# Kernel optimization log

Hardware: AMD Instinct MI355X
Metric: run time of the kernel (lower is better)

## Reference

```python
import jax, jax.numpy as jnp
import numpy as np

MAX_STEP = 20

def setup_inputs() -> dict:
    key = jax.random.key(0)
    k1, k2 = jax.random.split(key)
    B, L, E, H = 32, 2048, 256, 256
    word_rep = jax.random.normal(k1, (B, L, E), dtype=jnp.float32)
    # nn.Parameter(torch.randn(...).uniform_(-0.1, 0.1)) -> uniform in [-0.1, 0.1]
    cnn = jax.random.uniform(k2, (MAX_STEP, E, H), dtype=jnp.float32, minval=-0.1, maxval=0.1)
    return {"word_rep": word_rep, "cnn": cnn}

def reference(word_rep, cnn):
    # word_rep: [B, L, E]; cnn: [MAX_STEP, E, H]
    L = word_rep.shape[1]
    # Gather the cyclically-indexed per-position weight: [L, E, H]
    W = cnn[jnp.arange(L) % MAX_STEP]
    # Fused batched matmul over all positions at once: [B, L, H]
    hidden_vecs = jnp.einsum('ble,leh->blh', word_rep, W)
    return (hidden_vecs, hidden_vecs[:, -1])
```

## Files before the change

### kernel.cpp

```cpp
#include <hip/hip_runtime.h>
#include <hip/hip_bf16.h>

#define B_ 32
#define L_ 2048
#define E_ 256
#define H_ 256
#define MAXSTEP 20
#define NL 4
#define NCH 26
#define NGRP (MAXSTEP * NCH)

typedef __attribute__((ext_vector_type(4))) float f32x4;
typedef __attribute__((ext_vector_type(8))) short bf16x8;
using bf16 = __hip_bfloat16;

__device__ inline short cvt1(float x) {
    bf16 b = __float2bfloat16(x);
    return *reinterpret_cast<short*>(&b);
}

__global__ void transpose_w_kernel(const float* __restrict__ cnn, short* __restrict__ wt) {
    __shared__ short tile[32][33];
    const int s  = blockIdx.z;
    const int e0 = blockIdx.y * 32;
    const int h0 = blockIdx.x * 32;
    const int tx = threadIdx.x;
    const int ty = threadIdx.y;
    const float* src = cnn + ((size_t)s * E_ + e0) * H_ + h0;
#pragma unroll
    for (int i = ty; i < 32; i += 8)
        tile[i][tx] = cvt1(src[(size_t)i * H_ + tx]);
    __syncthreads();
    short* dst = wt + ((size_t)s * H_ + h0) * E_ + e0;
#pragma unroll
    for (int i = ty; i < 32; i += 8)
        dst[(size_t)i * E_ + tx] = tile[tx][i];
}

__global__ __launch_bounds__(512, 4) void vaw_occ_kernel(
        const float* __restrict__ A, const short* __restrict__ Wt,
        float* __restrict__ out) {
    __shared__ __align__(16) float aLds[2][B_ * E_];

    const int g_    = blockIdx.x;
    const int s     = g_ / NCH;
    const int chunk = g_ % NCH;
    const int cnt   = (s < 8) ? 103 : 102;
    const int wv    = threadIdx.x >> 6;
    const int lane  = threadIdx.x & 63;
    const int r     = lane & 15;
    const int g     = lane >> 4;
    const int nbase = wv * 32;
    const int key   = r & 7;

    auto lof = [&](int il) {
        int idx = chunk * NL + il;
        if (idx > cnt - 1) idx = cnt - 1;
        return s + 20 * idx;
    };

    auto stage = [&](int it) {
        const int l = lof(it);
        float* dst = aLds[it & 1];
#pragma unroll
        for (int j = 0; j < 4; ++j) {
            const int row = wv + j * 8;
            const int cg  = lane ^ (row & 7);
            const float* gp = A + ((size_t)row * L_ + l) * E_ + cg * 4;
            __builtin_amdgcn_global_load_lds(
                (const __attribute__((address_space(1))) void*)gp,
                (__attribute__((address_space(3))) void*)&dst[row * 256],
                16, 0, 0);
        }
    };

    stage(0);
    stage(1);

    const short* wtb = Wt + ((size_t)s * H_ + nbase + r) * E_ + g * 8;
    bf16x8 breg[8][2];
#pragma unroll
    for (int kk = 0; kk < 8; ++kk)
#pragma unroll
        for (int nf = 0; nf < 2; ++nf)
            breg[kk][nf] = *(const bf16x8*)(wtb + (size_t)nf * 16 * E_ + kk * 32);

#pragma unroll 1
    for (int it = 0; it < NL; ++it) {
        const int l   = lof(it);
        const int cur = it & 1;

        if (it < NL - 1 && it >= 1) stage(it + 1);

        if (it < NL - 1) asm volatile("s_waitcnt vmcnt(20)" ::: "memory");
        else             asm volatile("s_waitcnt vmcnt(16)" ::: "memory");
        __builtin_amdgcn_s_barrier();
        __builtin_amdgcn_sched_barrier(0);

        f32x4 acc[2][2];
#pragma unroll
        for (int mf = 0; mf < 2; ++mf)
#pragma unroll
            for (int nf = 0; nf < 2; ++nf)
                acc[mf][nf] = f32x4{0.f, 0.f, 0.f, 0.f};

#pragma unroll
        for (int kk = 0; kk < 8; ++kk) {
            const int c0 = kk * 8 + g * 2;
            f32x4 a0lo = *(const f32x4*)&aLds[cur][r * 256 + ((c0 ^ key) << 2)];
            f32x4 a0hi = *(const f32x4*)&aLds[cur][r * 256 + (((c0 + 1) ^ key) << 2)];
            f32x4 a1lo = *(const f32x4*)&aLds[cur][(r + 16) * 256 + ((c0 ^ key) << 2)];
            f32x4 a1hi = *(const f32x4*)&aLds[cur][(r + 16) * 256 + (((c0 + 1) ^ key) << 2)];
            bf16x8 a0, a1;
#pragma unroll
            for (int j = 0; j < 4; ++j) {
                a0[j]     = cvt1(a0lo[j]);
                a0[j + 4] = cvt1(a0hi[j]);
                a1[j]     = cvt1(a1lo[j]);
                a1[j + 4] = cvt1(a1hi[j]);
            }
#pragma unroll
            for (int nf = 0; nf < 2; ++nf) {
                acc[0][nf] = __builtin_amdgcn_mfma_f32_16x16x32_bf16(a0, breg[kk][nf], acc[0][nf], 0, 0, 0);
                acc[1][nf] = __builtin_amdgcn_mfma_f32_16x16x32_bf16(a1, breg[kk][nf], acc[1][nf], 0, 0, 0);
            }
        }

        const int row0 = g * 4;
#pragma unroll
        for (int mf = 0; mf < 2; ++mf) {
#pragma unroll
            for (int nf = 0; nf < 2; ++nf) {
                const int h = nbase + nf * 16 + r;
#pragma unroll
                for (int i = 0; i < 4; ++i) {
                    const int bb = mf * 16 + row0 + i;
                    out[((size_t)bb * L_ + l) * H_ + h] = acc[mf][nf][i];
                }
            }
        }
        if (l == L_ - 1) {
            float* out2 = out + (size_t)B_ * L_ * H_;
#pragma unroll
            for (int mf = 0; mf < 2; ++mf)
#pragma unroll
                for (int nf = 0; nf < 2; ++nf) {
                    const int h = nbase + nf * 16 + r;
#pragma unroll
                    for (int i = 0; i < 4; ++i) {
                        const int bb = mf * 16 + row0 + i;
                        out2[(size_t)bb * H_ + h] = acc[mf][nf][i];
                    }
                }
        }

        __builtin_amdgcn_s_barrier();
    }
}

__global__ __launch_bounds__(256) void vaw_fallback_kernel(
        const float* __restrict__ A, const float* __restrict__ W, float* __restrict__ out) {
    __shared__ __align__(16) float aLds[2][B_ * E_];
    const int l0   = blockIdx.x * 4;
    const int wv   = threadIdx.x >> 6;
    const int lane = threadIdx.x & 63;
    const int r    = lane & 15;
    const int g    = lane >> 4;
    const int nbase = wv * 64;
    const int key   = r & 7;

    auto stage = [&](int it) {
        float* dst = aLds[it & 1];
        const int l = l0 + it;
#pragma unroll
        for (int t = 0; t < 8; ++t) {
            const int b  = t * 4 + wv;
            const int cgx = lane ^ (b & 7);
            const float* gp = A + ((size_t)b * L_ + l) * E_ + cgx * 4;
            __builtin_amdgcn_global_load_lds(
                (const __attribute__((address_space(1))) void*)gp,
                (__attribute__((address_space(3))) void*)&dst[b * 256],
                16, 0, 0);
        }
    };

    stage(0);
#pragma unroll 1
    for (int it = 0; it < 4; ++it) {
        const int l   = l0 + it;
        const int sidx = l % MAXSTEP;
        const int cur = it & 1;
        if (it < 3) {
            stage(it + 1);
            asm volatile("s_waitcnt vmcnt(8)" ::: "memory");
        } else {
            asm volatile("s_waitcnt vmcnt(0)" ::: "memory");
        }
        __builtin_amdgcn_s_barrier();
        __builtin_amdgcn_sched_barrier(0);

        f32x4 acc[2][4] = {};
        const float* Wf = W + (size_t)sidx * E_ * H_;
#pragma unroll 2
        for (int kk = 0; kk < 8; ++kk) {
            const int k0 = kk * 32;
            const int c0 = kk * 8 + g * 2;
            f32x4 a0lo = *(const f32x4*)&aLds[cur][r * 256 + ((c0 ^ key) << 2)];
            f32x4 a0hi = *(const f32x4*)&aLds[cur][r * 256 + (((c0 + 1) ^ key) << 2)];
            f32x4 a1lo = *(const f32x4*)&aLds[cur][(r + 16) * 256 + ((c0 ^ key) << 2)];
            f32x4 a1hi = *(const f32x4*)&aLds[cur][(r + 16) * 256 + (((c0 + 1) ^ key) << 2)];
            bf16x8 a0, a1;
#pragma unroll
            for (int j = 0; j < 4; ++j) {
                a0[j]     = cvt1(a0lo[j]);
                a0[j + 4] = cvt1(a0hi[j]);
                a1[j]     = cvt1(a1lo[j]);
                a1[j + 4] = cvt1(a1hi[j]);
            }
            bf16x8 b0, b1, b2, b3;
#pragma unroll
            for (int j = 0; j < 8; ++j) {
                const size_t krow = (size_t)(k0 + g * 8 + j) * H_;
                b0[j] = cvt1(Wf[krow + nbase +  0 + r]);
                b1[j] = cvt1(Wf[krow + nbase + 16 + r]);
                b2[j] = cvt1(Wf[krow + nbase + 32 + r]);
                b3[j] = cvt1(Wf[krow + nbase + 48 + r]);
            }
            acc[0][0] = __builtin_amdgcn_mfma_f32_16x16x32_bf16(a0, b0, acc[0][0], 0, 0, 0);
            acc[0][1] = __builtin_amdgcn_mfma_f32_16x16x32_bf16(a0, b1, acc[0][1], 0, 0, 0);
            acc[0][2] = __builtin_amdgcn_mfma_f32_16x16x32_bf16(a0, b2, acc[0][2], 0, 0, 0);
            acc[0][3] = __builtin_amdgcn_mfma_f32_16x16x32_bf16(a0, b3, acc[0][3], 0, 0, 0);
            acc[1][0] = __builtin_amdgcn_mfma_f32_16x16x32_bf16(a1, b0, acc[1][0], 0, 0, 0);
            acc[1][1] = __builtin_amdgcn_mfma_f32_16x16x32_bf16(a1, b1, acc[1][1], 0, 0, 0);
            acc[1][2] = __builtin_amdgcn_mfma_f32_16x16x32_bf16(a1, b2, acc[1][2], 0, 0, 0);
            acc[1][3] = __builtin_amdgcn_mfma_f32_16x16x32_bf16(a1, b3, acc[1][3], 0, 0, 0);
        }

        const int row0 = g * 4;
#pragma unroll
        for (int mf = 0; mf < 2; ++mf)
#pragma unroll
            for (int nf = 0; nf < 4; ++nf) {
                const int h = nbase + nf * 16 + r;
#pragma unroll
                for (int i = 0; i < 4; ++i) {
                    const int bb = mf * 16 + row0 + i;
                    out[((size_t)bb * L_ + l) * H_ + h] = acc[mf][nf][i];
                }
            }
        if (l == L_ - 1) {
            float* out2 = out + (size_t)B_ * L_ * H_;
#pragma unroll
            for (int mf = 0; mf < 2; ++mf)
#pragma unroll
                for (int nf = 0; nf < 4; ++nf) {
                    const int h = nbase + nf * 16 + r;
#pragma unroll
                    for (int i = 0; i < 4; ++i) {
                        const int bb = mf * 16 + row0 + i;
                        out2[(size_t)bb * H_ + h] = acc[mf][nf][i];
                    }
                }
        }
        __builtin_amdgcn_s_barrier();
    }
}

extern "C" void kernel_launch(void* const* d_in, const int* in_sizes, int n_in,
                              void* d_out, int out_size, void* d_ws, size_t ws_size,
                              hipStream_t stream) {
    const float* word_rep = (const float*)d_in[0];
    const float* cnn      = (const float*)d_in[1];
    float* out = (float*)d_out;

    const size_t wt_bytes = (size_t)MAXSTEP * E_ * H_ * sizeof(short);
    if (ws_size >= wt_bytes) {
        short* wt = (short*)d_ws;
        transpose_w_kernel<<<dim3(8, 8, 20), dim3(32, 8), 0, stream>>>(cnn, wt);
        vaw_occ_kernel<<<dim3(NGRP), dim3(512), 0, stream>>>(word_rep, wt, out);
    } else {
        vaw_fallback_kernel<<<dim3(L_ / 4), dim3(256), 0, stream>>>(word_rep, cnn, out);
    }
}
```

Baseline: 55.85 us.

## Swap MFMA operands for vectorized output stores and use 4-wave blocks

Passes the weight fragment as the first MFMA operand and the activation as the second, so each lane's accumulator holds four consecutive H values and results can be written as 16-byte vector stores instead of scalar strided stores. Blocks shrink from 8 waves to 4, and each wave now covers 64 output columns, which doubles the weight registers held per wave. Weight register loads move ahead of the activation staging, and only one stage is issued up front, with prefetch of the next stage inside the loop. The trade-off is higher register pressure and fewer waves per block, in exchange for coalesced output writes.

```diff
diff --git a/kernel.cpp b/kernel.cpp
--- a/kernel.cpp
+++ b/kernel.cpp
@@ -37,7 +37,7 @@
         dst[(size_t)i * E_ + tx] = tile[tx][i];
 }
 
-__global__ __launch_bounds__(512, 4) void vaw_occ_kernel(
+__global__ __launch_bounds__(256, 2) void vaw_swap_kernel(
         const float* __restrict__ A, const short* __restrict__ Wt,
         float* __restrict__ out) {
     __shared__ __align__(16) float aLds[2][B_ * E_];
@@ -50,8 +50,16 @@
     const int lane  = threadIdx.x & 63;
     const int r     = lane & 15;
     const int g     = lane >> 4;
-    const int nbase = wv * 32;
+    const int nbase = wv * 64;
     const int key   = r & 7;
+
+    const short* wtb = Wt + ((size_t)s * H_ + nbase + r) * E_ + g * 8;
+    bf16x8 breg[8][4];
+#pragma unroll
+    for (int kk = 0; kk < 8; ++kk)
+#pragma unroll
+        for (int nf = 0; nf < 4; ++nf)
+            breg[kk][nf] = *(const bf16x8*)(wtb + (size_t)nf * 16 * E_ + kk * 32);
 
     auto lof = [&](int il) {
         int idx = chunk * NL + il;
@@ -63,46 +71,38 @@
         const int l = lof(it);
         float* dst = aLds[it & 1];
 #pragma unroll
-        for (int j = 0; j < 4; ++j) {
-            const int row = wv + j * 8;
-            const int cg  = lane ^ (row & 7);
-            const float* gp = A + ((size_t)row * L_ + l) * E_ + cg * 4;
+        for (int t = 0; t < 8; ++t) {
+            const int b  = t * 4 + wv;
+            const int cg = lane ^ (b & 7);
+            const float* gp = A + ((size_t)b * L_ + l) * E_ + cg * 4;
             __builtin_amdgcn_global_load_lds(
                 (const __attribute__((address_space(1))) void*)gp,
-                (__attribute__((address_space(3))) void*)&dst[row * 256],
+                (__attribute__((address_space(3))) void*)&dst[b * 256],
                 16, 0, 0);
         }
     };
 
     stage(0);
-    stage(1);
-
-    const short* wtb = Wt + ((size_t)s * H_ + nbase + r) * E_ + g * 8;
-    bf16x8 breg[8][2];
-#pragma unroll
-    for (int kk = 0; kk < 8; ++kk)
-#pragma unroll
-        for (int nf = 0; nf < 2; ++nf)
-            breg[kk][nf] = *(const bf16x8*)(wtb + (size_t)nf * 16 * E_ + kk * 32);
 
 #pragma unroll 1
     for (int it = 0; it < NL; ++it) {
         const int l   = lof(it);
         const int cur = it & 1;
 
-        if (it < NL - 1 && it >= 1) stage(it + 1);
-
-        if (it < NL - 1) asm volatile("s_waitcnt vmcnt(20)" ::: "memory");
-        else             asm volatile("s_waitcnt vmcnt(16)" ::: "memory");
+        if (it < NL - 1) stage(it + 1);
+
+        if (it == 0)          asm volatile("s_waitcnt vmcnt(8)"  ::: "memory");
+        else if (it < NL - 1) asm volatile("s_waitcnt vmcnt(16)" ::: "memory");
+        else                  asm volatile("s_waitcnt vmcnt(8)"  ::: "memory");
         __builtin_amdgcn_s_barrier();
         __builtin_amdgcn_sched_barrier(0);
 
-        f32x4 acc[2][2];
-#pragma unroll
-        for (int mf = 0; mf < 2; ++mf)
-#pragma unroll
-            for (int nf = 0; nf < 2; ++nf)
-                acc[mf][nf] = f32x4{0.f, 0.f, 0.f, 0.f};
+        f32x4 acc[4][2];
+#pragma unroll
+        for (int nf = 0; nf < 4; ++nf)
+#pragma unroll
+            for (int hf = 0; hf < 2; ++hf)
+                acc[nf][hf] = f32x4{0.f, 0.f, 0.f, 0.f};
 
 #pragma unroll
         for (int kk = 0; kk < 8; ++kk) {
@@ -120,38 +120,30 @@
                 a1[j + 4] = cvt1(a1hi[j]);
             }
 #pragma unroll
-            for (int nf = 0; nf < 2; ++nf) {
-                acc[0][nf] = __builtin_amdgcn_mfma_f32_16x16x32_bf16(a0, breg[kk][nf], acc[0][nf], 0, 0, 0);
-                acc[1][nf] = __builtin_amdgcn_mfma_f32_16x16x32_bf16(a1, breg[kk][nf], acc[1][nf], 0, 0, 0);
-            }
-        }
-
-        const int row0 = g * 4;
-#pragma unroll
-        for (int mf = 0; mf < 2; ++mf) {
-#pragma unroll
-            for (int nf = 0; nf < 2; ++nf) {
-                const int h = nbase + nf * 16 + r;
-#pragma unroll
-                for (int i = 0; i < 4; ++i) {
-                    const int bb = mf * 16 + row0 + i;
-                    out[((size_t)bb * L_ + l) * H_ + h] = acc[mf][nf][i];
-                }
-            }
+            for (int nf = 0; nf < 4; ++nf) {
+                acc[nf][0] = __builtin_amdgcn_mfma_f32_16x16x32_bf16(breg[kk][nf], a0, acc[nf][0], 0, 0, 0);
+                acc[nf][1] = __builtin_amdgcn_mfma_f32_16x16x32_bf16(breg[kk][nf], a1, acc[nf][1], 0, 0, 0);
+            }
+        }
+
+#pragma unroll
+        for (int hf = 0; hf < 2; ++hf) {
+            const int b = r + 16 * hf;
+            float* orow = out + ((size_t)b * L_ + l) * H_ + nbase + g * 4;
+#pragma unroll
+            for (int nf = 0; nf < 4; ++nf)
+                *(f32x4*)(orow + nf * 16) = acc[nf][hf];
         }
         if (l == L_ - 1) {
             float* out2 = out + (size_t)B_ * L_ * H_;
 #pragma unroll
-            for (int mf = 0; mf < 2; ++mf)
-#pragma unroll
-                for (int nf = 0; nf < 2; ++nf) {
-                    const int h = nbase + nf * 16 + r;
-#pragma unroll
-                    for (int i = 0; i < 4; ++i) {
-                        const int bb = mf * 16 + row0 + i;
-                        out2[(size_t)bb * H_ + h] = acc[mf][nf][i];
-                    }
-                }
+            for (int hf = 0; hf < 2; ++hf) {
+                const int b = r + 16 * hf;
+                float* orow = out2 + (size_t)b * H_ + nbase + g * 4;
+#pragma unroll
+                for (int nf = 0; nf < 4; ++nf)
+                    *(f32x4*)(orow + nf * 16) = acc[nf][hf];
+            }
         }
 
         __builtin_amdgcn_s_barrier();
@@ -277,7 +269,7 @@
     if (ws_size >= wt_bytes) {
         short* wt = (short*)d_ws;
         transpose_w_kernel<<<dim3(8, 8, 20), dim3(32, 8), 0, stream>>>(cnn, wt);
-        vaw_occ_kernel<<<dim3(NGRP), dim3(512), 0, stream>>>(word_rep, wt, out);
+        vaw_swap_kernel<<<dim3(NGRP), dim3(256), 0, stream>>>(word_rep, wt, out);
     } else {
         vaw_fallback_kernel<<<dim3(L_ / 4), dim3(256), 0, stream>>>(word_rep, cnn, out);
     }
```

New measurement: 46.72 us. 16.4% less time.
